# Kernel tuning notes

Measured on AMD Instinct MI355X. Metric: run time of the kernel, lower is better.

Reference implementation:

```python
import jax, jax.numpy as jnp
import numpy as np

N_NODES = 100000
N_EDGES = 3200000
NUM_FEATURES = 256
HIDDEN = 16
NUM_CLASSES = 40


def gcn_conv(x, edge_index, W, b, num_nodes):
    """PyG GCNConv: linear -> add self-loops -> symmetric deg norm -> scatter-add -> bias."""
    x = x @ W  # [N, out]
    loop = jnp.arange(num_nodes)
    src = jnp.concatenate([edge_index[0], loop])  # messages flow src -> dst
    dst = jnp.concatenate([edge_index[1], loop])
    # degree of target nodes (with self-loops)
    deg = jax.ops.segment_sum(jnp.ones_like(dst, dtype=x.dtype), dst,
                              num_segments=num_nodes)
    dinv = jnp.where(deg > 0, jax.lax.rsqrt(deg), 0.0)
    norm = dinv[src] * dinv[dst]  # [E+N]
    out = jax.ops.segment_sum(x[src] * norm[:, None], dst,
                              num_segments=num_nodes)
    return out + b


def setup_inputs() -> dict:
    key = jax.random.key(0)
    k1, k2, k3, k4 = jax.random.split(key, 4)
    x = jax.random.normal(k1, (N_NODES, NUM_FEATURES), dtype=jnp.float32)
    edge_index = jax.random.randint(k2, (2, N_EDGES), 0, N_NODES, dtype=jnp.int64)
    W1 = jax.random.normal(k3, (NUM_FEATURES, HIDDEN), dtype=jnp.float32) / np.sqrt(NUM_FEATURES)
    b1 = jnp.zeros((HIDDEN,), dtype=jnp.float32)
    W2 = jax.random.normal(k4, (HIDDEN, NUM_CLASSES), dtype=jnp.float32) / np.sqrt(HIDDEN)
    b2 = jnp.zeros((NUM_CLASSES,), dtype=jnp.float32)
    return {"x": x, "edge_index": edge_index, "W1": W1, "b1": b1, "W2": W2, "b2": b2}


def reference(x, edge_index, W1, b1, W2, b2):
    h = jax.nn.relu(gcn_conv(x, edge_index, W1, b1, N_NODES))
    return gcn_conv(h, edge_index, W2, b2, N_NODES)
```

## Files before the change

kernel.cpp:

```cpp
#include <hip/hip_runtime.h>
#include <hip/hip_fp16.h>

#define N_NODES   100000
#define N_EDGES   3200000
#define F_IN      256
#define HID       16
#define NCLS      40

#define CHUNK     16384
#define NBLK      ((N_EDGES + CHUNK - 1) / CHUNK)
#define B2SHIFT   9
#define NB2       ((N_NODES + 511) >> B2SHIFT)
#define BCAP      17408

__global__ __launch_bounds__(256) void hist_kernel(const int* __restrict__ ei,
                                                   int* __restrict__ hist_blk) {
    __shared__ int h[NB2];
    int blk = blockIdx.x, t = threadIdx.x;
    for (int i = t; i < NB2; i += 256) h[i] = 0;
    __syncthreads();
    int e0 = blk * CHUNK;
    int eN = min(CHUNK, N_EDGES - e0);
    const int4* d4 = (const int4*)(ei + N_EDGES + e0);
    for (int i = t; i < (eN >> 2); i += 256) {
        int4 d = d4[i];
        atomicAdd(&h[d.x >> B2SHIFT], 1);
        atomicAdd(&h[d.y >> B2SHIFT], 1);
        atomicAdd(&h[d.z >> B2SHIFT], 1);
        atomicAdd(&h[d.w >> B2SHIFT], 1);
    }
    __syncthreads();
    for (int i = t; i < NB2; i += 256) hist_blk[i * NBLK + blk] = h[i];
}

__global__ __launch_bounds__(256) void rowscan_kernel(int* __restrict__ hist_blk,
                                                      int* __restrict__ rowsum) {
    __shared__ int part[256];
    int b = blockIdx.x, t = threadIdx.x;
    int v = (t < NBLK) ? hist_blk[b * NBLK + t] : 0;
    part[t] = v;
    __syncthreads();
    for (int off = 1; off < 256; off <<= 1) {
        int u = (t >= off) ? part[t - off] : 0;
        __syncthreads();
        part[t] += u;
        __syncthreads();
    }
    if (t < NBLK) hist_blk[b * NBLK + t] = part[t] - v;
    if (t == 255) rowsum[b] = part[255];
}

__global__ __launch_bounds__(256) void bin2_kernel(const int* __restrict__ ei,
                                                   const int* __restrict__ hist_blk,
                                                   const int* __restrict__ rowsum,
                                                   int* __restrict__ buf) {
    __shared__ int cur[NB2];
    __shared__ int sc[256];
    int blk = blockIdx.x, t = threadIdx.x;
    int rv = (t < NB2) ? rowsum[t] : 0;
    sc[t] = rv;
    __syncthreads();
    for (int off = 1; off < 256; off <<= 1) {
        int u = (t >= off) ? sc[t - off] : 0;
        __syncthreads();
        sc[t] += u;
        __syncthreads();
    }
    if (t < NB2) cur[t] = (sc[t] - rv) + hist_blk[t * NBLK + blk];
    __syncthreads();
    int e0 = blk * CHUNK;
    int eN = min(CHUNK, N_EDGES - e0);
    const int4* s4 = (const int4*)(ei + e0);
    const int4* d4 = (const int4*)(ei + N_EDGES + e0);
    for (int i = t; i < (eN >> 2); i += 256) {
        int4 d = d4[i], s = s4[i];
        int p0 = atomicAdd(&cur[d.x >> B2SHIFT], 1); buf[p0] = ((d.x & 511) << 17) | s.x;
        int p1 = atomicAdd(&cur[d.y >> B2SHIFT], 1); buf[p1] = ((d.y & 511) << 17) | s.y;
        int p2 = atomicAdd(&cur[d.z >> B2SHIFT], 1); buf[p2] = ((d.z & 511) << 17) | s.z;
        int p3 = atomicAdd(&cur[d.w >> B2SHIFT], 1); buf[p3] = ((d.w & 511) << 17) | s.w;
    }
}

__global__ __launch_bounds__(512) void build_kernel(const int* __restrict__ buf,
                                                    const int* __restrict__ rowsum,
                                                    int* __restrict__ rowptr,
                                                    float* __restrict__ dinv,
                                                    int* __restrict__ csr_src) {
    __shared__ int lbuf[BCAP];
    __shared__ int hist[512], offs[512], cur[512];
    __shared__ int sc[256];
    int b = blockIdx.x, t = threadIdx.x;
    int rv = 0;
    if (t < 256) { rv = (t < NB2) ? rowsum[t] : 0; sc[t] = rv; }
    hist[t] = 0;
    __syncthreads();
    for (int off = 1; off < 256; off <<= 1) {
        int u = (t < 256 && t >= off) ? sc[t - off] : 0;
        __syncthreads();
        if (t < 256) sc[t] += u;
        __syncthreads();
    }
    int cnt  = rowsum[b];
    int base = sc[b] - cnt;
    for (int i = t; i < cnt; i += 512) {
        int v = buf[base + i];
        if (i < BCAP) lbuf[i] = v;
        atomicAdd(&hist[v >> 17], 1);
    }
    __syncthreads();
    int v = hist[t];
    offs[t] = v;
    __syncthreads();
    for (int off = 1; off < 512; off <<= 1) {
        int u = (t >= off) ? offs[t - off] : 0;
        __syncthreads();
        offs[t] += u;
        __syncthreads();
    }
    int ex = offs[t] - v;
    int n = (b << B2SHIFT) + t;
    if (n < N_NODES) {
        rowptr[n] = base + ex;
        dinv[n]   = rsqrtf((float)(v + 1));
    }
    if (b == 0 && t == 0) rowptr[N_NODES] = N_EDGES;
    cur[t] = ex;
    __syncthreads();
    for (int i = t; i < cnt; i += 512) {
        int p = (i < BCAP) ? lbuf[i] : buf[base + i];
        int pos = atomicAdd(&cur[p >> 17], 1);
        csr_src[base + pos] = p & 0x1FFFF;
    }
}

__global__ __launch_bounds__(256) void gemm1_kernel(const float* __restrict__ x,
                                                    const float* __restrict__ W1,
                                                    const float* __restrict__ dinv,
                                                    __half* __restrict__ y1h) {
    __shared__ float W1s[F_IN * HID];
    int t = threadIdx.x;
    #pragma unroll
    for (int i = 0; i < (F_IN * HID) / 256; i++) W1s[t + i * 256] = W1[t + i * 256];
    __syncthreads();

    int n0 = blockIdx.x * 512 + t;
    int n1 = n0 + 256;
    if (n0 >= N_NODES) return;
    bool v1 = (n1 < N_NODES);

    const float4* xr0 = (const float4*)(x + (size_t)n0 * F_IN);
    const float4* xr1 = (const float4*)(x + (size_t)(v1 ? n1 : n0) * F_IN);
    float acc0[HID], acc1[HID];
    #pragma unroll
    for (int h = 0; h < HID; h++) { acc0[h] = 0.f; acc1[h] = 0.f; }

    #pragma unroll 2
    for (int k4 = 0; k4 < F_IN / 4; k4++) {
        float4 xa = xr0[k4];
        float4 xb = xr1[k4];
        int k = k4 * 4;
        #pragma unroll
        for (int h = 0; h < HID; h++) {
            float w0 = W1s[(k + 0) * HID + h];
            float w1 = W1s[(k + 1) * HID + h];
            float w2 = W1s[(k + 2) * HID + h];
            float w3 = W1s[(k + 3) * HID + h];
            acc0[h] += xa.x * w0 + xa.y * w1 + xa.z * w2 + xa.w * w3;
            acc1[h] += xb.x * w0 + xb.y * w1 + xb.z * w2 + xb.w * w3;
        }
    }
    {
        float dv = dinv[n0];
        __half2 hp[8];
        #pragma unroll
        for (int j = 0; j < 8; j++)
            hp[j] = __float22half2_rn(make_float2(acc0[2 * j] * dv, acc0[2 * j + 1] * dv));
        float4* o = (float4*)(y1h + (size_t)n0 * HID);
        o[0] = ((float4*)hp)[0];
        o[1] = ((float4*)hp)[1];
    }
    if (v1) {
        float dv = dinv[n1];
        __half2 hp[8];
        #pragma unroll
        for (int j = 0; j < 8; j++)
            hp[j] = __float22half2_rn(make_float2(acc1[2 * j] * dv, acc1[2 * j + 1] * dv));
        float4* o = (float4*)(y1h + (size_t)n1 * HID);
        o[0] = ((float4*)hp)[0];
        o[1] = ((float4*)hp)[1];
    }
}

__device__ __forceinline__ void acc_row(const float4* __restrict__ tab, int s, float* acc) {
    float4 v0 = tab[(size_t)s * 2 + 0];
    float4 v1 = tab[(size_t)s * 2 + 1];
    const __half2* a0 = (const __half2*)&v0;
    const __half2* a1 = (const __half2*)&v1;
    #pragma unroll
    for (int j = 0; j < 4; j++) {
        float2 f0 = __half22float2(a0[j]);
        float2 f1 = __half22float2(a1[j]);
        acc[2 * j]         += f0.x;
        acc[2 * j + 1]     += f0.y;
        acc[8 + 2 * j]     += f1.x;
        acc[8 + 2 * j + 1] += f1.y;
    }
}

__device__ __forceinline__ void acc_row2(const float4* __restrict__ tab, int s0, int s1, float* acc) {
    float4 v0 = tab[(size_t)s0 * 2 + 0];
    float4 v1 = tab[(size_t)s0 * 2 + 1];
    float4 v2 = tab[(size_t)s1 * 2 + 0];
    float4 v3 = tab[(size_t)s1 * 2 + 1];
    const __half2* a0 = (const __half2*)&v0;
    const __half2* a1 = (const __half2*)&v1;
    const __half2* b0 = (const __half2*)&v2;
    const __half2* b1 = (const __half2*)&v3;
    #pragma unroll
    for (int j = 0; j < 4; j++) {
        float2 f0 = __half22float2(a0[j]);
        float2 f1 = __half22float2(a1[j]);
        float2 g0 = __half22float2(b0[j]);
        float2 g1 = __half22float2(b1[j]);
        acc[2 * j]         += f0.x + g0.x;
        acc[2 * j + 1]     += f0.y + g0.y;
        acc[8 + 2 * j]     += f1.x + g1.x;
        acc[8 + 2 * j + 1] += f1.y + g1.y;
    }
}

__global__ __launch_bounds__(256) void gather1_kernel(const int* __restrict__ rowptr,
                                                      const int* __restrict__ csr_src,
                                                      const __half* __restrict__ y1h,
                                                      const float* __restrict__ b1,
                                                      const float* __restrict__ dinv,
                                                      __half* __restrict__ zh) {
    int n   = blockIdx.x * 64 + (threadIdx.x >> 2);
    int sub = threadIdx.x & 3;
    if (n >= N_NODES) return;
    const float4* tab = (const float4*)y1h;
    int beg = rowptr[n], end = rowptr[n + 1];
    float acc[16];
    #pragma unroll
    for (int i = 0; i < 16; i++) acc[i] = 0.f;
    if (sub == 0) acc_row(tab, n, acc);
    int e = beg + sub;
    for (; e + 4 < end; e += 8)
        acc_row2(tab, csr_src[e], csr_src[e + 4], acc);
    if (e < end) acc_row(tab, csr_src[e], acc);
    #pragma unroll
    for (int m = 1; m < 4; m <<= 1) {
        #pragma unroll
        for (int i = 0; i < 16; i++) acc[i] += __shfl_xor(acc[i], m, 4);
    }
    if (sub < 2) {
        float dv = dinv[n];
        const float4* b1q = (const float4*)b1;
        float4 ba = b1q[sub * 2], bb = b1q[sub * 2 + 1];
        float bv[8] = {ba.x, ba.y, ba.z, ba.w, bb.x, bb.y, bb.z, bb.w};
        __half2 outp[4];
        #pragma unroll
        for (int j = 0; j < 4; j++) {
            float2 r;
            r.x = fmaxf(dv * acc[sub * 8 + 2 * j]     + bv[2 * j],     0.f) * dv;
            r.y = fmaxf(dv * acc[sub * 8 + 2 * j + 1] + bv[2 * j + 1], 0.f) * dv;
            outp[j] = __float22half2_rn(r);
        }
        *(float4*)(zh + (size_t)n * HID + sub * 8) = *(float4*)outp;
    }
}

__global__ __launch_bounds__(256) void gather2_kernel(const int* __restrict__ rowptr,
                                                      const int* __restrict__ csr_src,
                                                      const __half* __restrict__ zh,
                                                      const float* __restrict__ W2,
                                                      const float* __restrict__ b2,
                                                      const float* __restrict__ dinv,
                                                      float* __restrict__ out) {
    __shared__ float W2s[HID * NCLS];
    __shared__ float b2s[NCLS];
    int t = threadIdx.x;
    for (int i = t; i < HID * NCLS; i += 256) W2s[i] = W2[i];
    if (t < NCLS) b2s[t] = b2[t];
    __syncthreads();

    int n   = blockIdx.x * 64 + (t >> 2);
    int sub = t & 3;
    if (n >= N_NODES) return;
    const float4* tab = (const float4*)zh;
    int beg = rowptr[n], end = rowptr[n + 1];
    float acc[16];
    #pragma unroll
    for (int i = 0; i < 16; i++) acc[i] = 0.f;
    if (sub == 0) acc_row(tab, n, acc);
    int e = beg + sub;
    for (; e + 4 < end; e += 8)
        acc_row2(tab, csr_src[e], csr_src[e + 4], acc);
    if (e < end) acc_row(tab, csr_src[e], acc);
    #pragma unroll
    for (int m = 1; m < 4; m <<= 1) {
        #pragma unroll
        for (int i = 0; i < 16; i++) acc[i] += __shfl_xor(acc[i], m, 4);
    }
    float dv = dinv[n];
    int c0 = sub * 10;
    float o[10];
    #pragma unroll
    for (int j = 0; j < 10; j++) o[j] = 0.f;
    #pragma unroll
    for (int h = 0; h < HID; h++) {
        float a = acc[h];
        const float* w = &W2s[h * NCLS + c0];
        #pragma unroll
        for (int j = 0; j < 10; j++) o[j] += a * w[j];
    }
    float* op = out + (size_t)n * NCLS + c0;
    #pragma unroll
    for (int j = 0; j < 5; j++) {
        float2 r = make_float2(dv * o[2 * j]     + b2s[c0 + 2 * j],
                               dv * o[2 * j + 1] + b2s[c0 + 2 * j + 1]);
        *(float2*)(op + 2 * j) = r;
    }
}

extern "C" void kernel_launch(void* const* d_in, const int* in_sizes, int n_in,
                              void* d_out, int out_size, void* d_ws, size_t ws_size,
                              hipStream_t stream) {
    const float* x   = (const float*)d_in[0];
    const int*   ei  = (const int*)  d_in[1];
    const float* W1  = (const float*)d_in[2];
    const float* b1  = (const float*)d_in[3];
    const float* W2  = (const float*)d_in[4];
    const float* b2  = (const float*)d_in[5];
    float* out = (float*)d_out;

    char* ws = (char*)d_ws;
    size_t off = 0;
    int*   hist_blk = (int*)(ws + off); off += (size_t)NB2 * NBLK * 4;
    int*   rowsum   = (int*)(ws + off); off += (size_t)NB2 * 4;
    off = (off + 15) & ~(size_t)15;
    int*    rowptr  = (int*)   (ws + off); off += (size_t)(N_NODES + 1) * 4;
    off = (off + 15) & ~(size_t)15;
    float*  dinv    = (float*) (ws + off); off += (size_t)N_NODES * 4;
    int*    csr_src = (int*)   (ws + off); off += (size_t)N_EDGES * 4;
    int*    buf     = (int*)   (ws + off); off += (size_t)N_EDGES * 4;
    __half* y1h     = (__half*)(ws + off); off += (size_t)N_NODES * HID * 2;
    __half* zh      = (__half*)(ws + off); off += (size_t)N_NODES * HID * 2;

    hist_kernel    <<<NBLK, 256, 0, stream>>>(ei, hist_blk);
    rowscan_kernel <<<NB2, 256, 0, stream>>>(hist_blk, rowsum);
    bin2_kernel    <<<NBLK, 256, 0, stream>>>(ei, hist_blk, rowsum, buf);
    build_kernel   <<<NB2, 512, 0, stream>>>(buf, rowsum, rowptr, dinv, csr_src);

    gemm1_kernel  <<<(N_NODES + 511) / 512, 256, 0, stream>>>(x, W1, dinv, y1h);
    gather1_kernel<<<(N_NODES + 63) / 64, 256, 0, stream>>>(rowptr, csr_src, y1h, b1, dinv, zh);
    gather2_kernel<<<(N_NODES + 63) / 64, 256, 0, stream>>>(rowptr, csr_src, zh, W2, b2, dinv, out);
}
```

Before: 330.3 us.

## Fuse histogram with GEMM1, drop rowscan kernel, apply source dinv in gather

Result: slower. 337.4 us (+2.2%).

```diff
diff --git a/kernel.cpp b/kernel.cpp
--- a/kernel.cpp
+++ b/kernel.cpp
@@ -12,67 +12,99 @@
 #define B2SHIFT   9
 #define NB2       ((N_NODES + 511) >> B2SHIFT)
 #define BCAP      17408
-
-__global__ __launch_bounds__(256) void hist_kernel(const int* __restrict__ ei,
-                                                   int* __restrict__ hist_blk) {
-    __shared__ int h[NB2];
+#define K1_GRID   256
+#define NPB       391
+
+__global__ __launch_bounds__(512) void k1_hist_gemm(const int* __restrict__ ei,
+                                                    const float* __restrict__ x,
+                                                    const float* __restrict__ W1,
+                                                    int* __restrict__ hist_blk,
+                                                    __half* __restrict__ y1h) {
+    __shared__ float W1s[F_IN * HID];
+    int* h = (int*)W1s;
     int blk = blockIdx.x, t = threadIdx.x;
-    for (int i = t; i < NB2; i += 256) h[i] = 0;
-    __syncthreads();
-    int e0 = blk * CHUNK;
-    int eN = min(CHUNK, N_EDGES - e0);
-    const int4* d4 = (const int4*)(ei + N_EDGES + e0);
-    for (int i = t; i < (eN >> 2); i += 256) {
-        int4 d = d4[i];
-        atomicAdd(&h[d.x >> B2SHIFT], 1);
-        atomicAdd(&h[d.y >> B2SHIFT], 1);
-        atomicAdd(&h[d.z >> B2SHIFT], 1);
-        atomicAdd(&h[d.w >> B2SHIFT], 1);
-    }
-    __syncthreads();
-    for (int i = t; i < NB2; i += 256) hist_blk[i * NBLK + blk] = h[i];
-}
-
-__global__ __launch_bounds__(256) void rowscan_kernel(int* __restrict__ hist_blk,
-                                                      int* __restrict__ rowsum) {
-    __shared__ int part[256];
-    int b = blockIdx.x, t = threadIdx.x;
-    int v = (t < NBLK) ? hist_blk[b * NBLK + t] : 0;
-    part[t] = v;
-    __syncthreads();
-    for (int off = 1; off < 256; off <<= 1) {
-        int u = (t >= off) ? part[t - off] : 0;
-        __syncthreads();
-        part[t] += u;
-        __syncthreads();
-    }
-    if (t < NBLK) hist_blk[b * NBLK + t] = part[t] - v;
-    if (t == 255) rowsum[b] = part[255];
-}
-
-__global__ __launch_bounds__(256) void bin2_kernel(const int* __restrict__ ei,
-                                                   const int* __restrict__ hist_blk,
-                                                   const int* __restrict__ rowsum,
-                                                   int* __restrict__ buf) {
+
+    if (blk < NBLK) {
+        for (int i = t; i < NB2; i += 512) h[i] = 0;
+        __syncthreads();
+        int e0 = blk * CHUNK;
+        int eN = min(CHUNK, N_EDGES - e0);
+        const int4* d4 = (const int4*)(ei + N_EDGES + e0);
+        for (int i = t; i < (eN >> 2); i += 512) {
+            int4 d = d4[i];
+            atomicAdd(&h[d.x >> B2SHIFT], 1);
+            atomicAdd(&h[d.y >> B2SHIFT], 1);
+            atomicAdd(&h[d.z >> B2SHIFT], 1);
+            atomicAdd(&h[d.w >> B2SHIFT], 1);
+        }
+        __syncthreads();
+        for (int i = t; i < NB2; i += 512) hist_blk[i * NBLK + blk] = h[i];
+        __syncthreads();
+    }
+
+    #pragma unroll
+    for (int i = 0; i < (F_IN * HID) / 512; i++) W1s[t + i * 512] = W1[t + i * 512];
+    __syncthreads();
+
+    int n = blk * NPB + t;
+    if (t >= NPB || n >= N_NODES) return;
+
+    const float4* xr = (const float4*)(x + (size_t)n * F_IN);
+    float acc[HID];
+    #pragma unroll
+    for (int j = 0; j < HID; j++) acc[j] = 0.f;
+
+    #pragma unroll 4
+    for (int k4 = 0; k4 < F_IN / 4; k4++) {
+        float4 xv = xr[k4];
+        int k = k4 * 4;
+        #pragma unroll
+        for (int hh = 0; hh < HID; hh++) {
+            acc[hh] += xv.x * W1s[(k + 0) * HID + hh] + xv.y * W1s[(k + 1) * HID + hh]
+                     + xv.z * W1s[(k + 2) * HID + hh] + xv.w * W1s[(k + 3) * HID + hh];
+        }
+    }
+    __half2 hp[8];
+    #pragma unroll
+    for (int j = 0; j < 8; j++)
+        hp[j] = __float22half2_rn(make_float2(acc[2 * j], acc[2 * j + 1]));
+    float4* o = (float4*)(y1h + (size_t)n * HID);
+    o[0] = ((float4*)hp)[0];
+    o[1] = ((float4*)hp)[1];
+}
+
+__global__ __launch_bounds__(512) void k2_bin(const int* __restrict__ ei,
+                                              const int* __restrict__ hist_blk,
+                                              int* __restrict__ buf) {
     __shared__ int cur[NB2];
     __shared__ int sc[256];
     int blk = blockIdx.x, t = threadIdx.x;
-    int rv = (t < NB2) ? rowsum[t] : 0;
-    sc[t] = rv;
+    int pre = 0, tot = 0;
+    if (t < NB2) {
+        const int* row = hist_blk + t * NBLK;
+        for (int k = 0; k < NBLK; k++) {
+            int v = row[k];
+            pre += (k < blk) ? v : 0;
+            tot += v;
+        }
+    }
+    if (t < 256) sc[t] = tot;
     __syncthreads();
     for (int off = 1; off < 256; off <<= 1) {
-        int u = (t >= off) ? sc[t - off] : 0;
-        __syncthreads();
-        sc[t] += u;
-        __syncthreads();
-    }
-    if (t < NB2) cur[t] = (sc[t] - rv) + hist_blk[t * NBLK + blk];
-    __syncthreads();
+        int u = 0;
+        if (t < 256 && t >= off) u = sc[t - off];
+        __syncthreads();
+        if (t < 256) sc[t] += u;
+        __syncthreads();
+    }
+    if (t < NB2) cur[t] = (sc[t] - tot) + pre;
+    __syncthreads();
+
     int e0 = blk * CHUNK;
     int eN = min(CHUNK, N_EDGES - e0);
     const int4* s4 = (const int4*)(ei + e0);
     const int4* d4 = (const int4*)(ei + N_EDGES + e0);
-    for (int i = t; i < (eN >> 2); i += 256) {
+    for (int i = t; i < (eN >> 2); i += 512) {
         int4 d = d4[i], s = s4[i];
         int p0 = atomicAdd(&cur[d.x >> B2SHIFT], 1); buf[p0] = ((d.x & 511) << 17) | s.x;
         int p1 = atomicAdd(&cur[d.y >> B2SHIFT], 1); buf[p1] = ((d.y & 511) << 17) | s.y;
@@ -81,27 +113,36 @@
     }
 }
 
-__global__ __launch_bounds__(512) void build_kernel(const int* __restrict__ buf,
-                                                    const int* __restrict__ rowsum,
-                                                    int* __restrict__ rowptr,
-                                                    float* __restrict__ dinv,
-                                                    int* __restrict__ csr_src) {
+__global__ __launch_bounds__(512) void k3_build(const int* __restrict__ buf,
+                                               const int* __restrict__ hist_blk,
+                                               int* __restrict__ rowptr,
+                                               float* __restrict__ dinv,
+                                               int* __restrict__ csr_src) {
     __shared__ int lbuf[BCAP];
     __shared__ int hist[512], offs[512], cur[512];
     __shared__ int sc[256];
+    __shared__ int s_base, s_cnt;
     int b = blockIdx.x, t = threadIdx.x;
-    int rv = 0;
-    if (t < 256) { rv = (t < NB2) ? rowsum[t] : 0; sc[t] = rv; }
+
+    int tot = 0;
+    if (t < NB2) {
+        const int* row = hist_blk + t * NBLK;
+        for (int k = 0; k < NBLK; k++) tot += row[k];
+    }
+    if (t < 256) sc[t] = tot;
     hist[t] = 0;
     __syncthreads();
     for (int off = 1; off < 256; off <<= 1) {
-        int u = (t < 256 && t >= off) ? sc[t - off] : 0;
+        int u = 0;
+        if (t < 256 && t >= off) u = sc[t - off];
         __syncthreads();
         if (t < 256) sc[t] += u;
         __syncthreads();
     }
-    int cnt  = rowsum[b];
-    int base = sc[b] - cnt;
+    if (t == b) { s_base = sc[b] - tot; s_cnt = tot; }
+    __syncthreads();
+    int base = s_base, cnt = s_cnt;
+
     for (int i = t; i < cnt; i += 512) {
         int v = buf[base + i];
         if (i < BCAP) lbuf[i] = v;
@@ -133,61 +174,42 @@
     }
 }
 
-__global__ __launch_bounds__(256) void gemm1_kernel(const float* __restrict__ x,
-                                                    const float* __restrict__ W1,
-                                                    const float* __restrict__ dinv,
-                                                    __half* __restrict__ y1h) {
-    __shared__ float W1s[F_IN * HID];
-    int t = threadIdx.x;
-    #pragma unroll
-    for (int i = 0; i < (F_IN * HID) / 256; i++) W1s[t + i * 256] = W1[t + i * 256];
-    __syncthreads();
-
-    int n0 = blockIdx.x * 512 + t;
-    int n1 = n0 + 256;
-    if (n0 >= N_NODES) return;
-    bool v1 = (n1 < N_NODES);
-
-    const float4* xr0 = (const float4*)(x + (size_t)n0 * F_IN);
-    const float4* xr1 = (const float4*)(x + (size_t)(v1 ? n1 : n0) * F_IN);
-    float acc0[HID], acc1[HID];
-    #pragma unroll
-    for (int h = 0; h < HID; h++) { acc0[h] = 0.f; acc1[h] = 0.f; }
-
-    #pragma unroll 2
-    for (int k4 = 0; k4 < F_IN / 4; k4++) {
-        float4 xa = xr0[k4];
-        float4 xb = xr1[k4];
-        int k = k4 * 4;
-        #pragma unroll
-        for (int h = 0; h < HID; h++) {
-            float w0 = W1s[(k + 0) * HID + h];
-            float w1 = W1s[(k + 1) * HID + h];
-            float w2 = W1s[(k + 2) * HID + h];
-            float w3 = W1s[(k + 3) * HID + h];
-            acc0[h] += xa.x * w0 + xa.y * w1 + xa.z * w2 + xa.w * w3;
-            acc1[h] += xb.x * w0 + xb.y * w1 + xb.z * w2 + xb.w * w3;
-        }
-    }
-    {
-        float dv = dinv[n0];
-        __half2 hp[8];
-        #pragma unroll
-        for (int j = 0; j < 8; j++)
-            hp[j] = __float22half2_rn(make_float2(acc0[2 * j] * dv, acc0[2 * j + 1] * dv));
-        float4* o = (float4*)(y1h + (size_t)n0 * HID);
-        o[0] = ((float4*)hp)[0];
-        o[1] = ((float4*)hp)[1];
-    }
-    if (v1) {
-        float dv = dinv[n1];
-        __half2 hp[8];
-        #pragma unroll
-        for (int j = 0; j < 8; j++)
-            hp[j] = __float22half2_rn(make_float2(acc1[2 * j] * dv, acc1[2 * j + 1] * dv));
-        float4* o = (float4*)(y1h + (size_t)n1 * HID);
-        o[0] = ((float4*)hp)[0];
-        o[1] = ((float4*)hp)[1];
+__device__ __forceinline__ void acc_row_s(const float4* __restrict__ tab, int s, float w, float* acc) {
+    float4 v0 = tab[(size_t)s * 2 + 0];
+    float4 v1 = tab[(size_t)s * 2 + 1];
+    const __half2* a0 = (const __half2*)&v0;
+    const __half2* a1 = (const __half2*)&v1;
+    #pragma unroll
+    for (int j = 0; j < 4; j++) {
+        float2 f0 = __half22float2(a0[j]);
+        float2 f1 = __half22float2(a1[j]);
+        acc[2 * j]         += w * f0.x;
+        acc[2 * j + 1]     += w * f0.y;
+        acc[8 + 2 * j]     += w * f1.x;
+        acc[8 + 2 * j + 1] += w * f1.y;
+    }
+}
+
+__device__ __forceinline__ void acc_row2_s(const float4* __restrict__ tab, int s0, int s1,
+                                           float w0, float w1, float* acc) {
+    float4 v0 = tab[(size_t)s0 * 2 + 0];
+    float4 v1 = tab[(size_t)s0 * 2 + 1];
+    float4 v2 = tab[(size_t)s1 * 2 + 0];
+    float4 v3 = tab[(size_t)s1 * 2 + 1];
+    const __half2* a0 = (const __half2*)&v0;
+    const __half2* a1 = (const __half2*)&v1;
+    const __half2* b0 = (const __half2*)&v2;
+    const __half2* b1 = (const __half2*)&v3;
+    #pragma unroll
+    for (int j = 0; j < 4; j++) {
+        float2 f0 = __half22float2(a0[j]);
+        float2 f1 = __half22float2(a1[j]);
+        float2 g0 = __half22float2(b0[j]);
+        float2 g1 = __half22float2(b1[j]);
+        acc[2 * j]         += w0 * f0.x + w1 * g0.x;
+        acc[2 * j + 1]     += w0 * f0.y + w1 * g0.y;
+        acc[8 + 2 * j]     += w0 * f1.x + w1 * g1.x;
+        acc[8 + 2 * j + 1] += w0 * f1.y + w1 * g1.y;
     }
 }
 
@@ -239,22 +261,27 @@
     int sub = threadIdx.x & 3;
     if (n >= N_NODES) return;
     const float4* tab = (const float4*)y1h;
+    float dvn = dinv[n];
     int beg = rowptr[n], end = rowptr[n + 1];
     float acc[16];
     #pragma unroll
     for (int i = 0; i < 16; i++) acc[i] = 0.f;
-    if (sub == 0) acc_row(tab, n, acc);
+    if (sub == 0) acc_row_s(tab, n, dvn, acc);
     int e = beg + sub;
-    for (; e + 4 < end; e += 8)
-        acc_row2(tab, csr_src[e], csr_src[e + 4], acc);
-    if (e < end) acc_row(tab, csr_src[e], acc);
+    for (; e + 4 < end; e += 8) {
+        int s0 = csr_src[e], s1 = csr_src[e + 4];
+        acc_row2_s(tab, s0, s1, dinv[s0], dinv[s1], acc);
+    }
+    if (e < end) {
+        int s = csr_src[e];
+        acc_row_s(tab, s, dinv[s], acc);
+    }
     #pragma unroll
     for (int m = 1; m < 4; m <<= 1) {
         #pragma unroll
         for (int i = 0; i < 16; i++) acc[i] += __shfl_xor(acc[i], m, 4);
     }
     if (sub < 2) {
-        float dv = dinv[n];
         const float4* b1q = (const float4*)b1;
         float4 ba = b1q[sub * 2], bb = b1q[sub * 2 + 1];
         float bv[8] = {ba.x, ba.y, ba.z, ba.w, bb.x, bb.y, bb.z, bb.w};
@@ -262,8 +289,8 @@
         #pragma unroll
         for (int j = 0; j < 4; j++) {
             float2 r;
-            r.x = fmaxf(dv * acc[sub * 8 + 2 * j]     + bv[2 * j],     0.f) * dv;
-            r.y = fmaxf(dv * acc[sub * 8 + 2 * j + 1] + bv[2 * j + 1], 0.f) * dv;
+            r.x = fmaxf(dvn * acc[sub * 8 + 2 * j]     + bv[2 * j],     0.f) * dvn;
+            r.y = fmaxf(dvn * acc[sub * 8 + 2 * j + 1] + bv[2 * j + 1], 0.f) * dvn;
             outp[j] = __float22half2_rn(r);
         }
         *(float4*)(zh + (size_t)n * HID + sub * 8) = *(float4*)outp;
@@ -337,7 +364,6 @@
     char* ws = (char*)d_ws;
     size_t off = 0;
     int*   hist_blk = (int*)(ws + off); off += (size_t)NB2 * NBLK * 4;
-    int*   rowsum   = (int*)(ws + off); off += (size_t)NB2 * 4;
     off = (off + 15) & ~(size_t)15;
     int*    rowptr  = (int*)   (ws + off); off += (size_t)(N_NODES + 1) * 4;
     off = (off + 15) & ~(size_t)15;
@@ -347,12 +373,9 @@
     __half* y1h     = (__half*)(ws + off); off += (size_t)N_NODES * HID * 2;
     __half* zh      = (__half*)(ws + off); off += (size_t)N_NODES * HID * 2;
 
-    hist_kernel    <<<NBLK, 256, 0, stream>>>(ei, hist_blk);
-    rowscan_kernel <<<NB2, 256, 0, stream>>>(hist_blk, rowsum);
-    bin2_kernel    <<<NBLK, 256, 0, stream>>>(ei, hist_blk, rowsum, buf);
-    build_kernel   <<<NB2, 512, 0, stream>>>(buf, rowsum, rowptr, dinv, csr_src);
-
-    gemm1_kernel  <<<(N_NODES + 511) / 512, 256, 0, stream>>>(x, W1, dinv, y1h);
+    k1_hist_gemm <<<K1_GRID, 512, 0, stream>>>(ei, x, W1, hist_blk, y1h);
+    k2_bin       <<<NBLK, 512, 0, stream>>>(ei, hist_blk, buf);
+    k3_build     <<<NB2, 512, 0, stream>>>(buf, hist_blk, rowptr, dinv, csr_src);
     gather1_kernel<<<(N_NODES + 63) / 64, 256, 0, stream>>>(rowptr, csr_src, y1h, b1, dinv, zh);
     gather2_kernel<<<(N_NODES + 63) / 64, 256, 0, stream>>>(rowptr, csr_src, zh, W2, b2, dinv, out);
 }
```
